# Performance work log

Measured on AMD Instinct MI355X. Metric: run time of the kernel, lower is better.

The kernel has to match this reference:

```python
import jax, jax.numpy as jnp
import numpy as np

B, C, L = 8, 256, 2048
RED = 8
CQK = C // RED  # 32


def setup_inputs() -> dict:
    key = jax.random.key(0)
    ks = jax.random.split(key, 8)
    s = 0.05
    x = jax.random.normal(ks[0], (B, C, L), dtype=jnp.float32)
    Wq = jax.random.normal(ks[1], (CQK, C), dtype=jnp.float32) * s
    bq = jax.random.normal(ks[2], (CQK,), dtype=jnp.float32) * s
    Wk = jax.random.normal(ks[3], (CQK, C), dtype=jnp.float32) * s
    bk = jax.random.normal(ks[4], (CQK,), dtype=jnp.float32) * s
    Wv = jax.random.normal(ks[5], (C, C), dtype=jnp.float32) * s
    bv = jax.random.normal(ks[6], (C,), dtype=jnp.float32) * s
    gamma = jnp.asarray([0.5], dtype=jnp.float32)  # learned scalar (init 0 in torch)
    return {"x": x, "Wq": Wq, "bq": bq, "Wk": Wk, "bk": bk, "Wv": Wv, "bv": bv, "gamma": gamma}


def reference(x, Wq, bq, Wk, bk, Wv, bv, gamma):
    # 1x1 Conv1d == channel-mixing matmul: [O,C] x [B,C,L] -> [B,O,L]
    q = jnp.einsum('oc,bcl->bol', Wq, x) + bq[:, None]   # [B,CQK,L]
    k = jnp.einsum('oc,bcl->bol', Wk, x) + bk[:, None]   # [B,CQK,L]
    v = jnp.einsum('oc,bcl->bol', Wv, x) + bv[:, None]   # [B,C,L]
    # attn[b,i,j] = softmax_j( q(:,i) . k(:,j) )  -- NOTE: no 1/sqrt(d) scaling
    scores = jnp.einsum('bci,bcj->bij', q, k)            # [B,L,L]
    attn = jax.nn.softmax(scores, axis=-1)
    # out[b,c,i] = sum_j v[b,c,j] * attn[b,i,j]
    out = jnp.einsum('bcj,bij->bci', v, attn)            # [B,C,L]
    return gamma[0] * out + x
```

## Files before the change

kernel.cpp:

```cpp
#include <hip/hip_runtime.h>

#define B 8
#define C 256
#define L 2048
#define CQK 32
#define SSEG 4
#define JSEG (L / SSEG)
#define NT (JSEG / 32)
#define SM_SHIFT 20.0f

typedef unsigned short u16;
typedef __attribute__((ext_vector_type(8))) short bf8;
typedef __attribute__((ext_vector_type(4))) float f4;

__device__ __forceinline__ u16 f2bf(float f) {
    union { float f; unsigned u; } v; v.f = f;
    unsigned r = v.u + 0x7FFFu + ((v.u >> 16) & 1u);
    return (u16)(r >> 16);
}
__device__ __forceinline__ float bfl(unsigned u) {
    union { unsigned u; float f; } v; v.u = u << 16; return v.f;
}
__device__ __forceinline__ float bfh(unsigned u) {
    union { unsigned u; float f; } v; v.u = u & 0xFFFF0000u; return v.f;
}

__device__ __forceinline__ void gld16(const u16* gp, u16* lp) {
    auto* g1 = (const __attribute__((address_space(1))) u16*)gp;
    auto* l3 = (__attribute__((address_space(3))) u16*)lp;
    __builtin_amdgcn_global_load_lds(g1, l3, 16, 0, 0);
}
__device__ __forceinline__ void wait_vm0() {
    asm volatile("s_waitcnt vmcnt(0)" ::: "memory");
    __builtin_amdgcn_sched_barrier(0);
}
__device__ __forceinline__ void wait_lgkm0() {
    asm volatile("s_waitcnt lgkmcnt(0)" ::: "memory");
    __builtin_amdgcn_sched_barrier(0);
}
__device__ __forceinline__ void bar() {
    __builtin_amdgcn_sched_barrier(0);
    __builtin_amdgcn_s_barrier();
    __builtin_amdgcn_sched_barrier(0);
}

__global__ __launch_bounds__(256) void wconv(
    const float* __restrict__ Wq, const float* __restrict__ bq,
    const float* __restrict__ Wk, const float* __restrict__ bk,
    const float* __restrict__ Wv, const float* __restrict__ bv,
    u16* __restrict__ Wall, float* __restrict__ ball)
{
    const int idx = (blockIdx.x * 256 + threadIdx.x) * 4;
    const int row = idx >> 8, c = idx & 255;
    const float* s;
    if (row < 32)      s = Wq + row * C + c;
    else if (row < 64) s = Wk + (row - 32) * C + c;
    else               s = Wv + (row - 64) * C + c;
    const float4 v = *(const float4*)s;
    uint2 o;
    o.x = f2bf(v.x) | ((unsigned)f2bf(v.y) << 16);
    o.y = f2bf(v.z) | ((unsigned)f2bf(v.w) << 16);
    *(uint2*)(Wall + idx) = o;
    if (blockIdx.x == 0) {
        for (int i = threadIdx.x; i < 320; i += 256)
            ball[i] = (i < 32) ? bq[i] : (i < 64) ? bk[i - 32] : bv[i - 64];
    }
}

__global__ __launch_bounds__(256) void xconv(const float* __restrict__ x,
                                             u16* __restrict__ xt)
{
    __shared__ float tile[64][65];
    const int b = blockIdx.z, c0 = blockIdx.y * 64, l0 = blockIdx.x * 64;
    const int t = threadIdx.x;
    const int ln = t & 63, w = t >> 6;
#pragma unroll
    for (int i = 0; i < 16; i++) {
        const int c = w * 16 + i;
        tile[c][ln] = x[((size_t)(b * C + c0 + c)) * L + l0 + ln];
    }
    __syncthreads();
    const int lrow = t >> 2, q = t & 3;
    unsigned o[8];
#pragma unroll
    for (int jj = 0; jj < 8; jj++) {
        const float a0 = tile[q * 16 + jj * 2][lrow];
        const float a1 = tile[q * 16 + jj * 2 + 1][lrow];
        o[jj] = f2bf(a0) | ((unsigned)f2bf(a1) << 16);
    }
    u16* dst = xt + ((size_t)(b * L + l0 + lrow)) * 256 + c0 + q * 16;
    *(uint4*)(dst)     = make_uint4(o[0], o[1], o[2], o[3]);
    *(uint4*)(dst + 8) = make_uint4(o[4], o[5], o[6], o[7]);
}

__global__ __launch_bounds__(256) void proj(
    const u16* __restrict__ xt, const u16* __restrict__ Wall,
    const float* __restrict__ ball, u16* __restrict__ qt,
    u16* __restrict__ kt, u16* __restrict__ vv)
{
    __shared__ u16 xlds[64 * 256];
    const int b = blockIdx.y, l0 = blockIdx.x * 64;
    const int t = threadIdx.x, w = t >> 6, ln = t & 63;
    const int lc = ln & 15, g = ln >> 4;

#pragma unroll
    for (int mm = 0; mm < 8; mm++) {
        const int cg = t + mm * 256;
        const int lrow = cg >> 5, phys = cg & 31;
        const int logical = (phys & 24) | ((phys & 7) ^ (lrow & 7));
        gld16(xt + ((size_t)(b * L + l0 + lrow)) * 256 + logical * 8,
              xlds + (size_t)(w * 64 + mm * 256) * 8);
    }
    __syncthreads();

    f4 acc[5][4];
#pragma unroll
    for (int rt = 0; rt < 5; rt++) {
        const int row0 = (w * 5 + rt) * 16 + g * 4;
        const float4 bi = *(const float4*)(ball + row0);
#pragma unroll
        for (int ct = 0; ct < 4; ct++) {
            acc[rt][ct].x = bi.x; acc[rt][ct].y = bi.y;
            acc[rt][ct].z = bi.z; acc[rt][ct].w = bi.w;
        }
    }

#pragma unroll
    for (int k = 0; k < 8; k++) {
        bf8 bfr[4];
#pragma unroll
        for (int ct = 0; ct < 4; ct++) {
            const int lrow = ct * 16 + lc;
            const int lchunk = k * 4 + g;
            const int phys = (lchunk & 24) | ((lchunk & 7) ^ (lrow & 7));
            bfr[ct] = *(const bf8*)(xlds + (size_t)lrow * 256 + phys * 8);
        }
#pragma unroll
        for (int rt = 0; rt < 5; rt++) {
            const bf8 af = *(const bf8*)(Wall +
                (size_t)((w * 5 + rt) * 16 + lc) * 256 + k * 32 + g * 8);
#pragma unroll
            for (int ct = 0; ct < 4; ct++)
                acc[rt][ct] = __builtin_amdgcn_mfma_f32_16x16x32_bf16(
                    af, bfr[ct], acc[rt][ct], 0, 0, 0);
        }
    }

#pragma unroll
    for (int rt = 0; rt < 5; rt++) {
        const int rg = w * 5 + rt;
        const int row0 = rg * 16 + g * 4;
#pragma unroll
        for (int ct = 0; ct < 4; ct++) {
            const int l = l0 + ct * 16 + lc;
            const f4 a = acc[rt][ct];
            if (rg < 2) {
                uint2 o;
                o.x = f2bf(a.x) | ((unsigned)f2bf(a.y) << 16);
                o.y = f2bf(a.z) | ((unsigned)f2bf(a.w) << 16);
                *(uint2*)(qt + ((size_t)(b * L + l)) * 32 + row0) = o;
            } else if (rg < 4) {
                uint2 o;
                o.x = f2bf(a.x) | ((unsigned)f2bf(a.y) << 16);
                o.y = f2bf(a.z) | ((unsigned)f2bf(a.w) << 16);
                *(uint2*)(kt + ((size_t)(b * L + l)) * 32 + (row0 - 32)) = o;
            } else {
                const int c = row0 - 64;
                vv[((size_t)(b * C + c + 0)) * L + l] = f2bf(a.x);
                vv[((size_t)(b * C + c + 1)) * L + l] = f2bf(a.y);
                vv[((size_t)(b * C + c + 2)) * L + l] = f2bf(a.z);
                vv[((size_t)(b * C + c + 3)) * L + l] = f2bf(a.w);
            }
        }
    }
}

__global__ __launch_bounds__(256, 4) void attn(
    const u16* __restrict__ qt, const u16* __restrict__ kt,
    const u16* __restrict__ vv, u16* __restrict__ po,
    float* __restrict__ plsum)
{
    __shared__ u16 vs[2][8192];
    __shared__ u16 ps[64][40];
    __shared__ float fl[64];

    const int b = blockIdx.y, bx = blockIdx.x, sidx = blockIdx.z;
    const int t = threadIdx.x, w = t >> 6, ln = t & 63;
    const int lc = ln & 15, g = ln >> 4;
    const int i0 = bx * 64;
    const int js = sidx * JSEG;
    const int wc0 = w * 64;
    const int tb = (b * 32 + bx) * SSEG + sidx;

    const bf8 qf = *(const bf8*)(qt + ((size_t)(b * L + i0 + w * 16 + lc)) * 32 + g * 8);
    const u16* kbase = kt + ((size_t)b * L) * 32;

    f4 acc[4][4];
    const f4 fz = {0.f, 0.f, 0.f, 0.f};
#pragma unroll
    for (int it = 0; it < 4; it++)
#pragma unroll
        for (int ct = 0; ct < 4; ct++) acc[it][ct] = fz;
    float lsum = 0.f;

    auto stage_v = [&](int buf, int j0) {
#pragma unroll
        for (int mm = 0; mm < 4; mm++) {
            const int cg = t + mm * 256;
            const int c = cg >> 2, ch = cg & 3;
            gld16(vv + ((size_t)(b * C + c)) * L + j0 + ch * 8,
                  vs[buf] + (size_t)(w * 64 + mm * 256) * 8);
        }
    };

    stage_v(0, js);
    bf8 kf0 = *(const bf8*)(kbase + (size_t)(js + lc) * 32 + g * 8);
    bf8 kf1 = *(const bf8*)(kbase + (size_t)(js + 16 + lc) * 32 + g * 8);
    int cur = 0;

#pragma unroll 1
    for (int jt = 0; jt < NT; jt++) {
        wait_vm0();
        bar();
        if (jt + 1 < NT) stage_v(cur ^ 1, js + (jt + 1) * 32);
        bf8 kn0 = kf0, kn1 = kf1;
        if (jt + 1 < NT) {
            const int jn = js + (jt + 1) * 32;
            kn0 = *(const bf8*)(kbase + (size_t)(jn + lc) * 32 + g * 8);
            kn1 = *(const bf8*)(kbase + (size_t)(jn + 16 + lc) * 32 + g * 8);
        }

        const f4 s0 = __builtin_amdgcn_mfma_f32_16x16x32_bf16(kf0, qf, fz, 0, 0, 0);
        const f4 s1 = __builtin_amdgcn_mfma_f32_16x16x32_bf16(kf1, qf, fz, 0, 0, 0);

        const float p0 = __expf(s0.x - SM_SHIFT);
        const float p1 = __expf(s0.y - SM_SHIFT);
        const float p2 = __expf(s0.z - SM_SHIFT);
        const float p3 = __expf(s0.w - SM_SHIFT);
        const float p4 = __expf(s1.x - SM_SHIFT);
        const float p5 = __expf(s1.y - SM_SHIFT);
        const float p6 = __expf(s1.z - SM_SHIFT);
        const float p7 = __expf(s1.w - SM_SHIFT);
        {
            uint2 o;
            o.x = f2bf(p0) | ((unsigned)f2bf(p1) << 16);
            o.y = f2bf(p2) | ((unsigned)f2bf(p3) << 16);
            *(uint2*)(&ps[w * 16 + lc][g * 4]) = o;
            o.x = f2bf(p4) | ((unsigned)f2bf(p5) << 16);
            o.y = f2bf(p6) | ((unsigned)f2bf(p7) << 16);
            *(uint2*)(&ps[w * 16 + lc][16 + g * 4]) = o;
        }
        float psum = ((p0 + p1) + (p2 + p3)) + ((p4 + p5) + (p6 + p7));

        wait_lgkm0();
        bar();

        bf8 vfr[4];
#pragma unroll
        for (int ct = 0; ct < 4; ct++)
            vfr[ct] = *(const bf8*)(vs[cur] + (size_t)(wc0 + ct * 16 + lc) * 32 + g * 8);
        __builtin_amdgcn_s_setprio(1);
#pragma unroll
        for (int it = 0; it < 4; it++) {
            const bf8 paf = *(const bf8*)(&ps[it * 16 + lc][0] + g * 8);
#pragma unroll
            for (int ct = 0; ct < 4; ct++)
                acc[it][ct] = __builtin_amdgcn_mfma_f32_16x16x32_bf16(
                    paf, vfr[ct], acc[it][ct], 0, 0, 0);
        }
        __builtin_amdgcn_s_setprio(0);

        psum += __shfl_xor(psum, 16);
        psum += __shfl_xor(psum, 32);
        lsum += psum;

        kf0 = kn0; kf1 = kn1;
        cur ^= 1;
    }

    fl[w * 16 + lc] = 1.0f / lsum;
    if (g == 0) plsum[(size_t)tb * 64 + w * 16 + lc] = lsum;
    wait_lgkm0();
    bar();
    u16* pob = po + ((size_t)tb * 2048 + t) * 8;
#pragma unroll
    for (int it = 0; it < 4; it++) {
        const float4 iv = *(const float4*)&fl[it * 16 + g * 4];
#pragma unroll
        for (int cp = 0; cp < 2; cp++) {
            const f4 a0 = acc[it][2 * cp];
            const f4 a1 = acc[it][2 * cp + 1];
            uint4 o;
            o.x = f2bf(a0.x * iv.x) | ((unsigned)f2bf(a0.y * iv.y) << 16);
            o.y = f2bf(a0.z * iv.z) | ((unsigned)f2bf(a0.w * iv.w) << 16);
            o.z = f2bf(a1.x * iv.x) | ((unsigned)f2bf(a1.y * iv.y) << 16);
            o.w = f2bf(a1.z * iv.z) | ((unsigned)f2bf(a1.w * iv.w) << 16);
            *(uint4*)(pob + (size_t)(it * 2 + cp) * 2048) = o;
        }
    }
}

__global__ __launch_bounds__(256) void combine(
    const u16* __restrict__ po, const float* __restrict__ plsum,
    const float* __restrict__ x, const float* __restrict__ gamma_p,
    float* __restrict__ out)
{
    __shared__ float raw[4][16];
    __shared__ float wts[4][16];
    const int bx = blockIdx.x, b = blockIdx.y, z = blockIdx.z;
    const int t = threadIdx.x, wq = t >> 6, ln = t & 63;
    const int lc = ln & 15, g = ln >> 4;
    const int tbase = (b * 32 + bx) * SSEG;

    if (t < 64)
        raw[t >> 4][t & 15] = plsum[(size_t)(tbase + (t >> 4)) * 64 + z * 16 + (t & 15)];
    __syncthreads();
    if (t < 16) {
        const float l0 = raw[0][t], l1 = raw[1][t], l2 = raw[2][t], l3 = raw[3][t];
        const float inv = 1.0f / (((l0 + l1) + (l2 + l3)));
        wts[0][t] = l0 * inv; wts[1][t] = l1 * inv;
        wts[2][t] = l2 * inv; wts[3][t] = l3 * inv;
    }
    __syncthreads();

    f4 tot[4];
    const f4 fz = {0.f, 0.f, 0.f, 0.f};
#pragma unroll
    for (int ct = 0; ct < 4; ct++) tot[ct] = fz;

#pragma unroll
    for (int s = 0; s < SSEG; s++) {
        const u16* base = po + ((size_t)(tbase + s) * 2048 + (size_t)z * 2 * 256 + t) * 8;
        const uint4 q0 = *(const uint4*)base;
        const uint4 q1 = *(const uint4*)(base + 2048);
        const float4 wv = *(const float4*)&wts[s][g * 4];
        tot[0].x += wv.x * bfl(q0.x); tot[0].y += wv.y * bfh(q0.x);
        tot[0].z += wv.z * bfl(q0.y); tot[0].w += wv.w * bfh(q0.y);
        tot[1].x += wv.x * bfl(q0.z); tot[1].y += wv.y * bfh(q0.z);
        tot[1].z += wv.z * bfl(q0.w); tot[1].w += wv.w * bfh(q0.w);
        tot[2].x += wv.x * bfl(q1.x); tot[2].y += wv.y * bfh(q1.x);
        tot[2].z += wv.z * bfl(q1.y); tot[2].w += wv.w * bfh(q1.y);
        tot[3].x += wv.x * bfl(q1.z); tot[3].y += wv.y * bfh(q1.z);
        tot[3].z += wv.z * bfl(q1.w); tot[3].w += wv.w * bfh(q1.w);
    }

    const float gmm = gamma_p[0];
#pragma unroll
    for (int ct = 0; ct < 4; ct++) {
        const int c = wq * 64 + ct * 16 + lc;
        const size_t adr = ((size_t)(b * C + c)) * L + bx * 64 + z * 16 + g * 4;
        const float4 xv = *(const float4*)(x + adr);
        float4 o;
        o.x = gmm * tot[ct].x + xv.x;
        o.y = gmm * tot[ct].y + xv.y;
        o.z = gmm * tot[ct].z + xv.z;
        o.w = gmm * tot[ct].w + xv.w;
        *(float4*)(out + adr) = o;
    }
}

extern "C" void kernel_launch(void* const* d_in, const int* in_sizes, int n_in,
                              void* d_out, int out_size, void* d_ws, size_t ws_size,
                              hipStream_t stream) {
    const float* x  = (const float*)d_in[0];
    const float* Wq = (const float*)d_in[1];
    const float* bq = (const float*)d_in[2];
    const float* Wk = (const float*)d_in[3];
    const float* bk = (const float*)d_in[4];
    const float* Wv = (const float*)d_in[5];
    const float* bv = (const float*)d_in[6];
    const float* gm = (const float*)d_in[7];
    float* out = (float*)d_out;

    u16* vvp  = (u16*)d_ws;
    u16* qtp  = vvp + (size_t)B * C * L;
    u16* ktp  = qtp + (size_t)B * L * CQK;
    u16* Wall = ktp + (size_t)B * L * CQK;
    float* ball = (float*)(Wall + 320 * 256);
    u16* xt   = Wall + 320 * 256 + 640;
    u16* po   = xt;
    float* plsum = (float*)(po + (size_t)B * 32 * SSEG * 2048 * 8);

    wconv<<<80, 256, 0, stream>>>(Wq, bq, Wk, bk, Wv, bv, Wall, ball);
    xconv<<<dim3(L / 64, C / 64, B), 256, 0, stream>>>(x, xt);
    proj<<<dim3(L / 64, B), 256, 0, stream>>>(xt, Wall, ball, qtp, ktp, vvp);
    attn<<<dim3(L / 64, B, SSEG), 256, 0, stream>>>(qtp, ktp, vvp, po, plsum);
    combine<<<dim3(L / 64, B, SSEG), 256, 0, stream>>>(po, plsum, x, gm, out);
}
```

Baseline: 72.11 us.

## Load V fragments directly from global memory and double-buffer P tile

Drops the LDS staging of V through global_load_lds and its per-iteration vmcnt wait plus first barrier. Each wave now reads its own V fragments straight from global memory into registers at the top of the loop. The P scratch tile is double-buffered so only one barrier per iteration is needed. This removes an LDS round trip and one barrier, but V reads are no longer cooperatively coalesced and global load latency now sits on the MFMA critical path.

```diff
diff --git a/kernel.cpp b/kernel.cpp
--- a/kernel.cpp
+++ b/kernel.cpp
@@ -29,10 +29,6 @@
     auto* g1 = (const __attribute__((address_space(1))) u16*)gp;
     auto* l3 = (__attribute__((address_space(3))) u16*)lp;
     __builtin_amdgcn_global_load_lds(g1, l3, 16, 0, 0);
-}
-__device__ __forceinline__ void wait_vm0() {
-    asm volatile("s_waitcnt vmcnt(0)" ::: "memory");
-    __builtin_amdgcn_sched_barrier(0);
 }
 __device__ __forceinline__ void wait_lgkm0() {
     asm volatile("s_waitcnt lgkmcnt(0)" ::: "memory");
@@ -180,8 +176,7 @@
     const u16* __restrict__ vv, u16* __restrict__ po,
     float* __restrict__ plsum)
 {
-    __shared__ u16 vs[2][8192];
-    __shared__ u16 ps[64][40];
+    __shared__ u16 ps[2][64][40];
     __shared__ float fl[64];
 
     const int b = blockIdx.y, bx = blockIdx.x, sidx = blockIdx.z;
@@ -193,7 +188,8 @@
     const int tb = (b * 32 + bx) * SSEG + sidx;
 
     const bf8 qf = *(const bf8*)(qt + ((size_t)(b * L + i0 + w * 16 + lc)) * 32 + g * 8);
-    const u16* kbase = kt + ((size_t)b * L) * 32;
+    const u16* kb = kt + ((size_t)b * L) * 32 + (size_t)lc * 32 + g * 8;
+    const u16* vb = vv + ((size_t)(b * C + wc0 + lc)) * L + js + g * 8;
 
     f4 acc[4][4];
     const f4 fz = {0.f, 0.f, 0.f, 0.f};
@@ -203,35 +199,25 @@
         for (int ct = 0; ct < 4; ct++) acc[it][ct] = fz;
     float lsum = 0.f;
 
-    auto stage_v = [&](int buf, int j0) {
-#pragma unroll
-        for (int mm = 0; mm < 4; mm++) {
-            const int cg = t + mm * 256;
-            const int c = cg >> 2, ch = cg & 3;
-            gld16(vv + ((size_t)(b * C + c)) * L + j0 + ch * 8,
-                  vs[buf] + (size_t)(w * 64 + mm * 256) * 8);
-        }
-    };
-
-    stage_v(0, js);
-    bf8 kf0 = *(const bf8*)(kbase + (size_t)(js + lc) * 32 + g * 8);
-    bf8 kf1 = *(const bf8*)(kbase + (size_t)(js + 16 + lc) * 32 + g * 8);
+    bf8 kf0 = *(const bf8*)(kb + (size_t)(js) * 32);
+    bf8 kf1 = *(const bf8*)(kb + (size_t)(js + 16) * 32);
     int cur = 0;
 
 #pragma unroll 1
     for (int jt = 0; jt < NT; jt++) {
-        wait_vm0();
-        bar();
-        if (jt + 1 < NT) stage_v(cur ^ 1, js + (jt + 1) * 32);
-        bf8 kn0 = kf0, kn1 = kf1;
-        if (jt + 1 < NT) {
-            const int jn = js + (jt + 1) * 32;
-            kn0 = *(const bf8*)(kbase + (size_t)(jn + lc) * 32 + g * 8);
-            kn1 = *(const bf8*)(kbase + (size_t)(jn + 16 + lc) * 32 + g * 8);
-        }
+        bf8 vfr[4];
+#pragma unroll
+        for (int ct = 0; ct < 4; ct++)
+            vfr[ct] = *(const bf8*)(vb + (size_t)ct * 16 * L + jt * 32);
 
         const f4 s0 = __builtin_amdgcn_mfma_f32_16x16x32_bf16(kf0, qf, fz, 0, 0, 0);
         const f4 s1 = __builtin_amdgcn_mfma_f32_16x16x32_bf16(kf1, qf, fz, 0, 0, 0);
+
+        if (jt + 1 < NT) {
+            const size_t jn = (size_t)(js + (jt + 1) * 32);
+            kf0 = *(const bf8*)(kb + jn * 32);
+            kf1 = *(const bf8*)(kb + (jn + 16) * 32);
+        }
 
         const float p0 = __expf(s0.x - SM_SHIFT);
         const float p1 = __expf(s0.y - SM_SHIFT);
@@ -245,24 +231,20 @@
             uint2 o;
             o.x = f2bf(p0) | ((unsigned)f2bf(p1) << 16);
             o.y = f2bf(p2) | ((unsigned)f2bf(p3) << 16);
-            *(uint2*)(&ps[w * 16 + lc][g * 4]) = o;
+            *(uint2*)(&ps[cur][w * 16 + lc][g * 4]) = o;
             o.x = f2bf(p4) | ((unsigned)f2bf(p5) << 16);
             o.y = f2bf(p6) | ((unsigned)f2bf(p7) << 16);
-            *(uint2*)(&ps[w * 16 + lc][16 + g * 4]) = o;
+            *(uint2*)(&ps[cur][w * 16 + lc][16 + g * 4]) = o;
         }
         float psum = ((p0 + p1) + (p2 + p3)) + ((p4 + p5) + (p6 + p7));
 
         wait_lgkm0();
         bar();
 
-        bf8 vfr[4];
-#pragma unroll
-        for (int ct = 0; ct < 4; ct++)
-            vfr[ct] = *(const bf8*)(vs[cur] + (size_t)(wc0 + ct * 16 + lc) * 32 + g * 8);
         __builtin_amdgcn_s_setprio(1);
 #pragma unroll
         for (int it = 0; it < 4; it++) {
-            const bf8 paf = *(const bf8*)(&ps[it * 16 + lc][0] + g * 8);
+            const bf8 paf = *(const bf8*)(&ps[cur][it * 16 + lc][0] + g * 8);
 #pragma unroll
             for (int ct = 0; ct < 4; ct++)
                 acc[it][ct] = __builtin_amdgcn_mfma_f32_16x16x32_bf16(
@@ -274,7 +256,6 @@
         psum += __shfl_xor(psum, 32);
         lsum += psum;
 
-        kf0 = kn0; kf1 = kn1;
         cur ^= 1;
     }
 
```

Result: slower. 82.07 us (+13.8%).
